# Optimization experiments

Hardware: AMD Instinct MI355X
Metric: run time of the kernel (lower is better)

The kernel has to match this reference:

```python
import jax, jax.numpy as jnp
import numpy as np

B, N, M, H = 32, 1024, 256, 128


def setup_inputs() -> dict:
    key = jax.random.key(0)
    kA, kh, kW1, kW2 = jax.random.split(key, 4)
    A = jax.random.uniform(kA, (B, N, N), dtype=jnp.float32)
    h = jax.random.normal(kh, (B, N, M), dtype=jnp.float32)
    # torch Linear default init scale ~ 1/sqrt(fan_in)
    W1 = jax.random.normal(kW1, (M, H), dtype=jnp.float32) / np.sqrt(M)
    b1 = jnp.zeros((H,), dtype=jnp.float32)
    W2 = jax.random.normal(kW2, (H, M), dtype=jnp.float32) / np.sqrt(H)
    b2 = jnp.zeros((M,), dtype=jnp.float32)
    return {"A": A, "h": h, "W1": W1, "b1": b1, "W2": W2, "b2": b2}


def reference(A, h, W1, b1, W2, b2):
    # k = bmm(A, h) / 3 : [B,N,M]
    k = jnp.einsum('bij,bjm->bim', A, h) / 3.0
    # eta_g: Linear -> ReLU -> Linear
    k = jax.nn.relu(k @ W1 + b1) @ W2 + b2
    # A_mask = max over last dim of A, keepdims -> [B,N,1]
    A_mask = jnp.max(A, axis=-1, keepdims=True)
    # gated combine: k*mask + h*(mask-1)*(-1) == k*mask + h*(1-mask)
    return k * A_mask + h * (1.0 - A_mask)
```

## Files before the change

kernel.cpp:

```cpp
#include <hip/hip_runtime.h>

typedef __attribute__((ext_vector_type(8))) short bf16x8;
typedef __attribute__((ext_vector_type(4))) float f32x4;
typedef __attribute__((ext_vector_type(8))) unsigned short u16x8;

#define BB 32
#define NN 1024
#define MM 256
#define HH 128

__device__ __forceinline__ unsigned short f2bf(float f) {
  union { float f; unsigned int u; } c; c.f = f;
  unsigned int u = c.u + 0x7fffu + ((c.u >> 16) & 1u);
  return (unsigned short)(u >> 16);
}

__device__ __forceinline__ unsigned int cvtpk(float lo, float hi) {
  unsigned int r;
  asm("v_cvt_pk_bf16_f32 %0, %1, %2" : "=v"(r) : "v"(lo), "v"(hi));
  return r;
}

__device__ __forceinline__ float4 gload_f4(const float* p) {
  float4 r;
  asm volatile("global_load_dwordx4 %0, %1, off" : "=v"(r) : "v"(p) : "memory");
  return r;
}

typedef __attribute__((address_space(3))) unsigned int as3_u32;
typedef const __attribute__((address_space(1))) unsigned int as1_u32;
__device__ __forceinline__ void gl_lds16(const void* g, void* l) {
  __builtin_amdgcn_global_load_lds((as1_u32*)g, (as3_u32*)l, 16, 0, 0);
}

__global__ __launch_bounds__(256)
void k_transpose_h(const float* __restrict__ hg, unsigned short* __restrict__ hTg) {
  __shared__ unsigned short tile[64][65];
  int bid = blockIdx.x;
  int b = bid >> 6;
  int t = bid & 63;
  int k0 = (t >> 2) << 6;
  int m0 = (t & 3) << 6;
  int tt = threadIdx.x;
  {
    int r = tt >> 2;
    int cg = (tt & 3) << 4;
    const float* src = hg + (((size_t)b * NN + k0 + r) * MM + m0 + cg);
#pragma unroll
    for (int i = 0; i < 4; ++i) {
      float4 v = reinterpret_cast<const float4*>(src)[i];
      tile[r][cg + i * 4 + 0] = f2bf(v.x);
      tile[r][cg + i * 4 + 1] = f2bf(v.y);
      tile[r][cg + i * 4 + 2] = f2bf(v.z);
      tile[r][cg + i * 4 + 3] = f2bf(v.w);
    }
  }
  __syncthreads();
  {
    int mr = tt >> 2;
    int kc = (tt & 3) << 4;
    alignas(16) unsigned short tmp[16];
#pragma unroll
    for (int i = 0; i < 16; ++i) tmp[i] = tile[kc + i][mr];
    unsigned short* dst = hTg + (((size_t)b * MM + m0 + mr) * NN + k0 + kc);
    *reinterpret_cast<u16x8*>(dst)     = *reinterpret_cast<u16x8*>(tmp);
    *reinterpret_cast<u16x8*>(dst + 8) = *reinterpret_cast<u16x8*>(tmp + 8);
  }
}

__global__ __launch_bounds__(256)
void k_transpose_w(const float* __restrict__ W1, const float* __restrict__ W2,
                   unsigned short* __restrict__ W1T, unsigned short* __restrict__ W2T) {
  int idx = blockIdx.x * 256 + threadIdx.x;
  if (idx < MM * HH) {
    int hc = idx >> 8;
    int m  = idx & 255;
    W1T[idx] = f2bf(W1[m * HH + hc]);
  } else {
    int j = idx - MM * HH;
    int m  = j >> 7;
    int hd = j & 127;
    W2T[j] = f2bf(W2[hd * MM + m]);
  }
}

#define AB0 0
#define AB1 16384
#define HB0 32768
#define HB1 65536
#define KLD 0
#define CLD 65536

#define PIPE_BARRIER() do { \
  asm volatile("s_waitcnt lgkmcnt(0)" ::: "memory"); \
  __builtin_amdgcn_s_barrier(); \
  asm volatile("" ::: "memory"); } while (0)

#define VMWAIT0() do { \
  asm volatile("s_waitcnt vmcnt(0)" ::: "memory"); \
  __builtin_amdgcn_sched_barrier(0); } while (0)

__global__ __launch_bounds__(512, 1)
void k_fused(const float* __restrict__ Ag, const float* __restrict__ hg,
             const unsigned short* __restrict__ hTg,
             const unsigned short* __restrict__ W1Tg,
             const unsigned short* __restrict__ W2Tg,
             const float* __restrict__ b1g, const float* __restrict__ b2g,
             float* __restrict__ outg) {
  __shared__ __align__(16) char smem[98304];
  __shared__ float smax[128];

  const int tid  = threadIdx.x;
  const int lane = tid & 63;
  const int wid  = tid >> 6;
  const int wr   = wid >> 2;
  const int wc   = wid & 3;
  const int l15  = lane & 15;
  const int lg   = lane >> 4;

  const int bid = blockIdx.x;
  const int b   = bid & 31;
  const int r0  = (bid >> 5) << 7;

  const float* Ab = Ag + ((size_t)b * NN + r0) * NN;
  const unsigned short* hTb = hTg + (size_t)b * MM * NN;

  const int arow = tid >> 2;
  const int acg  = (tid & 3) << 4;
  const int asw  = (arow & 7) << 4;
  const float* Asrc = Ab + (size_t)arow * NN + acg;

  const unsigned short* baseH[4];
#pragma unroll
  for (int i = 0; i < 4; ++i) {
    int c = i * 512 + tid;
    int col = c >> 3, cic = c & 7;
    baseH[i] = hTb + (size_t)col * NN + ((cic ^ (col & 7)) << 3);
  }
  const int ldsW = wid << 10;

#define STAGE_H(K0, HB)                                                     \
  do {                                                                      \
    _Pragma("unroll")                                                       \
    for (int i = 0; i < 4; ++i)                                             \
      gl_lds16(baseH[i] + (K0), smem + (HB) + ldsW + i * 8192);             \
  } while (0)

  float4 rA[4];
#define ISSUE_A(K0)                                                         \
  do {                                                                      \
    _Pragma("unroll")                                                       \
    for (int i = 0; i < 4; ++i) rA[i] = gload_f4(Asrc + (K0) + i * 4);      \
  } while (0)

  float pmax = -1e30f;
#define CVTWR(AB)                                                           \
  do {                                                                      \
    float m0 = fmaxf(fmaxf(rA[0].x, rA[0].y), fmaxf(rA[0].z, rA[0].w));     \
    float m1 = fmaxf(fmaxf(rA[1].x, rA[1].y), fmaxf(rA[1].z, rA[1].w));     \
    float m2 = fmaxf(fmaxf(rA[2].x, rA[2].y), fmaxf(rA[2].z, rA[2].w));     \
    float m3 = fmaxf(fmaxf(rA[3].x, rA[3].y), fmaxf(rA[3].z, rA[3].w));     \
    pmax = fmaxf(pmax, fmaxf(fmaxf(m0, m1), fmaxf(m2, m3)));                \
    uint4 q0 = make_uint4(cvtpk(rA[0].x, rA[0].y), cvtpk(rA[0].z, rA[0].w), \
                          cvtpk(rA[1].x, rA[1].y), cvtpk(rA[1].z, rA[1].w));\
    uint4 q1 = make_uint4(cvtpk(rA[2].x, rA[2].y), cvtpk(rA[2].z, rA[2].w), \
                          cvtpk(rA[3].x, rA[3].y), cvtpk(rA[3].z, rA[3].w));\
    *reinterpret_cast<uint4*>(smem + (AB) + arow * 128 + ((acg * 2) ^ asw)) = q0; \
    *reinterpret_cast<uint4*>(smem + (AB) + arow * 128 + ((acg * 2 + 16) ^ asw)) = q1; \
  } while (0)

  f32x4 acc[4][4];
#pragma unroll
  for (int m = 0; m < 4; ++m)
#pragma unroll
    for (int n = 0; n < 4; ++n) acc[m][n] = f32x4{0.f, 0.f, 0.f, 0.f};

#define CONSUME(AB, HB)                                                     \
  do {                                                                      \
    _Pragma("unroll")                                                       \
    for (int kk = 0; kk < 2; ++kk) {                                        \
      const int kb = (kk * 32 + (lg << 3)) * 2;                             \
      bf16x8 af[4], bh[4];                                                  \
      _Pragma("unroll")                                                     \
      for (int m = 0; m < 4; ++m) {                                         \
        int row = (wr << 6) + (m << 4) + l15;                               \
        af[m] = *reinterpret_cast<const bf16x8*>(                           \
            smem + (AB) + row * 128 + (kb ^ ((row & 7) << 4)));             \
      }                                                                     \
      _Pragma("unroll")                                                     \
      for (int n = 0; n < 4; ++n) {                                         \
        int col = (wc << 6) + (n << 4) + l15;                               \
        bh[n] = *reinterpret_cast<const bf16x8*>(                           \
            smem + (HB) + col * 128 + (kb ^ ((col & 7) << 4)));             \
      }                                                                     \
      _Pragma("unroll")                                                     \
      for (int m = 0; m < 4; ++m)                                           \
        _Pragma("unroll")                                                   \
        for (int n = 0; n < 4; ++n)                                         \
          acc[m][n] = __builtin_amdgcn_mfma_f32_16x16x32_bf16(af[m], bh[n], \
                                                              acc[m][n], 0, 0, 0); \
    }                                                                       \
  } while (0)

  ISSUE_A(0);
  STAGE_H(0, HB0);
  VMWAIT0();
  CVTWR(AB0);
  PIPE_BARRIER();

#pragma unroll
  for (int t = 0; t < 16; ++t) {
    if (t < 15) {
      ISSUE_A((t + 1) * 64);
      STAGE_H((t + 1) * 64, (t & 1) ? HB0 : HB1);
    }
    if (t & 1) CONSUME(AB1, HB1);
    else       CONSUME(AB0, HB0);
    if (t < 15) {
      VMWAIT0();
      if (t & 1) CVTWR(AB0);
      else       CVTWR(AB1);
      PIPE_BARRIER();
    }
  }

  {
    float v = pmax;
    v = fmaxf(v, __shfl_xor(v, 1));
    v = fmaxf(v, __shfl_xor(v, 2));
    if ((tid & 3) == 0) smax[arow] = v;
  }
  __syncthreads();

  {
    const float inv3 = 1.0f / 3.0f;
#pragma unroll
    for (int m = 0; m < 4; ++m)
#pragma unroll
      for (int n = 0; n < 4; ++n) {
        int col = (wc << 6) + (n << 4) + l15;
#pragma unroll
        for (int j = 0; j < 4; ++j) {
          int row = (wr << 6) + (m << 4) + (lg << 2) + j;
          *reinterpret_cast<unsigned short*>(smem + KLD + row * 512 +
                                             ((col * 2) ^ ((row & 7) << 4))) =
              f2bf(acc[m][n][j] * inv3);
        }
      }
  }
  __syncthreads();

  f32x4 acc1[4][2];
#pragma unroll
  for (int m = 0; m < 4; ++m)
#pragma unroll
    for (int n = 0; n < 2; ++n) acc1[m][n] = f32x4{0.f, 0.f, 0.f, 0.f};
  const int wcol1 = wc << 5;
#pragma unroll
  for (int kq = 0; kq < 8; ++kq) {
    bf16x8 af[4], bw[2];
#pragma unroll
    for (int m = 0; m < 4; ++m) {
      int row = (wr << 6) + (m << 4) + l15;
      af[m] = *reinterpret_cast<const bf16x8*>(smem + KLD + row * 512 +
              (((kq * 32 + (lg << 3)) * 2) ^ ((row & 7) << 4)));
    }
#pragma unroll
    for (int n = 0; n < 2; ++n) {
      int col = wcol1 + (n << 4) + l15;
      bw[n] = *reinterpret_cast<const bf16x8*>(W1Tg + (size_t)col * 256 +
                                               kq * 32 + (lg << 3));
    }
#pragma unroll
    for (int m = 0; m < 4; ++m)
#pragma unroll
      for (int n = 0; n < 2; ++n)
        acc1[m][n] = __builtin_amdgcn_mfma_f32_16x16x32_bf16(af[m], bw[n], acc1[m][n], 0, 0, 0);
  }

  {
#pragma unroll
    for (int n = 0; n < 2; ++n) {
      int col = wcol1 + (n << 4) + l15;
      float bias = b1g[col];
#pragma unroll
      for (int m = 0; m < 4; ++m)
#pragma unroll
        for (int j = 0; j < 4; ++j) {
          int row = (wr << 6) + (m << 4) + (lg << 2) + j;
          float v = fmaxf(acc1[m][n][j] + bias, 0.f);
          *reinterpret_cast<unsigned short*>(smem + CLD + row * 256 +
                                             ((col * 2) ^ ((row & 7) << 4))) = f2bf(v);
        }
    }
  }
  __syncthreads();

  f32x4 acc2[4][4];
#pragma unroll
  for (int m = 0; m < 4; ++m)
#pragma unroll
    for (int n = 0; n < 4; ++n) acc2[m][n] = f32x4{0.f, 0.f, 0.f, 0.f};
#pragma unroll
  for (int kq = 0; kq < 4; ++kq) {
    bf16x8 af[4], bw[4];
#pragma unroll
    for (int m = 0; m < 4; ++m) {
      int row = (wr << 6) + (m << 4) + l15;
      af[m] = *reinterpret_cast<const bf16x8*>(smem + CLD + row * 256 +
              (((kq * 32 + (lg << 3)) * 2) ^ ((row & 7) << 4)));
    }
#pragma unroll
    for (int n = 0; n < 4; ++n) {
      int col = (wc << 6) + (n << 4) + l15;
      bw[n] = *reinterpret_cast<const bf16x8*>(W2Tg + (size_t)col * 128 +
                                               kq * 32 + (lg << 3));
    }
#pragma unroll
    for (int m = 0; m < 4; ++m)
#pragma unroll
      for (int n = 0; n < 4; ++n)
        acc2[m][n] = __builtin_amdgcn_mfma_f32_16x16x32_bf16(af[m], bw[n], acc2[m][n], 0, 0, 0);
  }

  {
#pragma unroll
    for (int n = 0; n < 4; ++n) {
      int col = (wc << 6) + (n << 4) + l15;
      float b2v = b2g[col];
#pragma unroll
      for (int m = 0; m < 4; ++m)
#pragma unroll
        for (int j = 0; j < 4; ++j) {
          int row = (wr << 6) + (m << 4) + (lg << 2) + j;
          float kv = acc2[m][n][j] + b2v;
          float mask = smax[row];
          size_t gidx = ((size_t)b * NN + r0 + row) * MM + col;
          float hv = hg[gidx];
          outg[gidx] = kv * mask + hv * (1.f - mask);
        }
    }
  }
#undef CONSUME
#undef CVTWR
#undef ISSUE_A
#undef STAGE_H
}

extern "C" void kernel_launch(void* const* d_in, const int* in_sizes, int n_in,
                              void* d_out, int out_size, void* d_ws, size_t ws_size,
                              hipStream_t stream) {
  (void)in_sizes; (void)n_in; (void)out_size; (void)ws_size;
  const float* A  = (const float*)d_in[0];
  const float* h  = (const float*)d_in[1];
  const float* W1 = (const float*)d_in[2];
  const float* b1 = (const float*)d_in[3];
  const float* W2 = (const float*)d_in[4];
  const float* b2 = (const float*)d_in[5];
  float* out = (float*)d_out;

  unsigned short* hT  = (unsigned short*)d_ws;
  unsigned short* W1T = (unsigned short*)((char*)d_ws + (size_t)BB * MM * NN * 2);
  unsigned short* W2T = W1T + MM * HH;

  k_transpose_h<<<BB * 64, 256, 0, stream>>>(h, hT);
  k_transpose_w<<<256, 256, 0, stream>>>(W1, W2, W1T, W2T);
  k_fused<<<BB * 8, 512, 0, stream>>>(A, h, hT, W1T, W2T, b1, b2, out);
}
```

Baseline: 69.36 us.

## Halve K-tile, shrink LDS, two-stage register prefetch of A, merge prep kernels

The main GEMM loop now uses 32-wide K tiles instead of 64, which shrinks the LDS footprint from 96KB to 64KB and aliases the epilogue buffers onto offset 0. A is prefetched into two alternating register sets, so loads run two tiles ahead under partial vmcnt waits. The h and W transpose kernels are merged into a single launch, and the memory clobber is dropped from the asm global load. The aim is more latency hiding and one fewer launch, at the cost of twice as many barriers per K and an extra sync before the epilogue reuses LDS.

```diff
diff --git a/kernel.cpp b/kernel.cpp
--- a/kernel.cpp
+++ b/kernel.cpp
@@ -14,19 +14,16 @@
   unsigned int u = c.u + 0x7fffu + ((c.u >> 16) & 1u);
   return (unsigned short)(u >> 16);
 }
-
 __device__ __forceinline__ unsigned int cvtpk(float lo, float hi) {
   unsigned int r;
   asm("v_cvt_pk_bf16_f32 %0, %1, %2" : "=v"(r) : "v"(lo), "v"(hi));
   return r;
 }
-
 __device__ __forceinline__ float4 gload_f4(const float* p) {
   float4 r;
-  asm volatile("global_load_dwordx4 %0, %1, off" : "=v"(r) : "v"(p) : "memory");
+  asm volatile("global_load_dwordx4 %0, %1, off" : "=v"(r) : "v"(p));
   return r;
 }
-
 typedef __attribute__((address_space(3))) unsigned int as3_u32;
 typedef const __attribute__((address_space(1))) unsigned int as1_u32;
 __device__ __forceinline__ void gl_lds16(const void* g, void* l) {
@@ -34,80 +31,76 @@
 }
 
 __global__ __launch_bounds__(256)
-void k_transpose_h(const float* __restrict__ hg, unsigned short* __restrict__ hTg) {
-  __shared__ unsigned short tile[64][65];
+void k_prep(const float* __restrict__ hg, unsigned short* __restrict__ hTg,
+            const float* __restrict__ W1, const float* __restrict__ W2,
+            unsigned short* __restrict__ W1T, unsigned short* __restrict__ W2T) {
   int bid = blockIdx.x;
-  int b = bid >> 6;
-  int t = bid & 63;
-  int k0 = (t >> 2) << 6;
-  int m0 = (t & 3) << 6;
-  int tt = threadIdx.x;
-  {
-    int r = tt >> 2;
-    int cg = (tt & 3) << 4;
-    const float* src = hg + (((size_t)b * NN + k0 + r) * MM + m0 + cg);
-#pragma unroll
-    for (int i = 0; i < 4; ++i) {
-      float4 v = reinterpret_cast<const float4*>(src)[i];
-      tile[r][cg + i * 4 + 0] = f2bf(v.x);
-      tile[r][cg + i * 4 + 1] = f2bf(v.y);
-      tile[r][cg + i * 4 + 2] = f2bf(v.z);
-      tile[r][cg + i * 4 + 3] = f2bf(v.w);
-    }
-  }
-  __syncthreads();
-  {
-    int mr = tt >> 2;
-    int kc = (tt & 3) << 4;
-    alignas(16) unsigned short tmp[16];
-#pragma unroll
-    for (int i = 0; i < 16; ++i) tmp[i] = tile[kc + i][mr];
-    unsigned short* dst = hTg + (((size_t)b * MM + m0 + mr) * NN + k0 + kc);
-    *reinterpret_cast<u16x8*>(dst)     = *reinterpret_cast<u16x8*>(tmp);
-    *reinterpret_cast<u16x8*>(dst + 8) = *reinterpret_cast<u16x8*>(tmp + 8);
-  }
-}
-
-__global__ __launch_bounds__(256)
-void k_transpose_w(const float* __restrict__ W1, const float* __restrict__ W2,
-                   unsigned short* __restrict__ W1T, unsigned short* __restrict__ W2T) {
-  int idx = blockIdx.x * 256 + threadIdx.x;
-  if (idx < MM * HH) {
-    int hc = idx >> 8;
-    int m  = idx & 255;
-    W1T[idx] = f2bf(W1[m * HH + hc]);
+  if (bid < BB * 64) {
+    __shared__ unsigned short tile[64][65];
+    int b = bid >> 6;
+    int t = bid & 63;
+    int k0 = (t >> 2) << 6;
+    int m0 = (t & 3) << 6;
+    int tt = threadIdx.x;
+    {
+      int r = tt >> 2;
+      int cg = (tt & 3) << 4;
+      const float* src = hg + (((size_t)b * NN + k0 + r) * MM + m0 + cg);
+#pragma unroll
+      for (int i = 0; i < 4; ++i) {
+        float4 v = reinterpret_cast<const float4*>(src)[i];
+        tile[r][cg + i * 4 + 0] = f2bf(v.x);
+        tile[r][cg + i * 4 + 1] = f2bf(v.y);
+        tile[r][cg + i * 4 + 2] = f2bf(v.z);
+        tile[r][cg + i * 4 + 3] = f2bf(v.w);
+      }
+    }
+    __syncthreads();
+    {
+      int mr = tt >> 2;
+      int kc = (tt & 3) << 4;
+      alignas(16) unsigned short tmp[16];
+#pragma unroll
+      for (int i = 0; i < 16; ++i) tmp[i] = tile[kc + i][mr];
+      unsigned short* dst = hTg + (((size_t)b * MM + m0 + mr) * NN + k0 + kc);
+      *reinterpret_cast<u16x8*>(dst)     = *reinterpret_cast<u16x8*>(tmp);
+      *reinterpret_cast<u16x8*>(dst + 8) = *reinterpret_cast<u16x8*>(tmp + 8);
+    }
   } else {
-    int j = idx - MM * HH;
-    int m  = j >> 7;
-    int hd = j & 127;
-    W2T[j] = f2bf(W2[hd * MM + m]);
-  }
-}
-
-#define AB0 0
-#define AB1 16384
-#define HB0 32768
-#define HB1 65536
+    int idx = (bid - BB * 64) * 256 + threadIdx.x;
+    if (idx < MM * HH) {
+      int hc = idx >> 8;
+      int m  = idx & 255;
+      W1T[idx] = f2bf(W1[m * HH + hc]);
+    } else {
+      int j = idx - MM * HH;
+      int m  = j >> 7;
+      int hd = j & 127;
+      W2T[j] = f2bf(W2[hd * MM + m]);
+    }
+  }
+}
+
+#define AB_(x) ((x) * 8192)
+#define HB_(x) (16384 + (x) * 16384)
 #define KLD 0
-#define CLD 65536
+#define CLD 0
 
 #define PIPE_BARRIER() do { \
   asm volatile("s_waitcnt lgkmcnt(0)" ::: "memory"); \
   __builtin_amdgcn_s_barrier(); \
   asm volatile("" ::: "memory"); } while (0)
-
-#define VMWAIT0() do { \
-  asm volatile("s_waitcnt vmcnt(0)" ::: "memory"); \
+#define VMW(N) do { asm volatile("s_waitcnt vmcnt(" #N ")" ::: "memory"); \
   __builtin_amdgcn_sched_barrier(0); } while (0)
 
-__global__ __launch_bounds__(512, 1)
+__global__ __launch_bounds__(512, 4)
 void k_fused(const float* __restrict__ Ag, const float* __restrict__ hg,
              const unsigned short* __restrict__ hTg,
              const unsigned short* __restrict__ W1Tg,
              const unsigned short* __restrict__ W2Tg,
              const float* __restrict__ b1g, const float* __restrict__ b2g,
              float* __restrict__ outg) {
-  __shared__ __align__(16) char smem[98304];
+  __shared__ __align__(16) char smem[65536];
   __shared__ float smax[128];
 
   const int tid  = threadIdx.x;
@@ -126,100 +119,96 @@
   const unsigned short* hTb = hTg + (size_t)b * MM * NN;
 
   const int arow = tid >> 2;
-  const int acg  = (tid & 3) << 4;
-  const int asw  = (arow & 7) << 4;
-  const float* Asrc = Ab + (size_t)arow * NN + acg;
-
-  const unsigned short* baseH[4];
-#pragma unroll
-  for (int i = 0; i < 4; ++i) {
-    int c = i * 512 + tid;
-    int col = c >> 3, cic = c & 7;
-    baseH[i] = hTb + (size_t)col * NN + ((cic ^ (col & 7)) << 3);
-  }
-  const int ldsW = wid << 10;
-
-#define STAGE_H(K0, HB)                                                     \
-  do {                                                                      \
-    _Pragma("unroll")                                                       \
-    for (int i = 0; i < 4; ++i)                                             \
-      gl_lds16(baseH[i] + (K0), smem + (HB) + ldsW + i * 8192);             \
+  const int ass  = tid & 3;
+  const float* Asrc = Ab + (size_t)arow * NN + (ass << 3);
+  const int awb = arow * 64 + ((ass << 4) ^ ((arow & 3) << 4));
+
+  const unsigned short* baseH[2];
+  {
+    int c0 = tid;
+    baseH[0] = hTb + (size_t)(c0 >> 2) * NN + (((c0 & 3) ^ ((c0 >> 2) & 3)) << 3);
+    int c1 = tid + 512;
+    baseH[1] = hTb + (size_t)(c1 >> 2) * NN + (((c1 & 3) ^ ((c1 >> 2) & 3)) << 3);
+  }
+  const int dstW = wid << 10;
+
+#define STAGE_H(K0, HB)                                                      \
+  do {                                                                       \
+    gl_lds16(baseH[0] + (K0), smem + (HB) + dstW);                           \
+    gl_lds16(baseH[1] + (K0), smem + (HB) + 8192 + dstW);                    \
   } while (0)
 
-  float4 rA[4];
-#define ISSUE_A(K0)                                                         \
-  do {                                                                      \
-    _Pragma("unroll")                                                       \
-    for (int i = 0; i < 4; ++i) rA[i] = gload_f4(Asrc + (K0) + i * 4);      \
+  float4 xa0, xa1, ya0, ya1;
+#define ISSUE_AX(K0) do { xa0 = gload_f4(Asrc + (K0)); \
+                          xa1 = gload_f4(Asrc + (K0) + 4); } while (0)
+#define ISSUE_AY(K0) do { ya0 = gload_f4(Asrc + (K0)); \
+                          ya1 = gload_f4(Asrc + (K0) + 4); } while (0)
+
+  float pmax = -1e30f;
+#define CVTWR(AB, R0, R1)                                                    \
+  do {                                                                       \
+    pmax = fmaxf(pmax, fmaxf(fmaxf(fmaxf((R0).x, (R0).y), fmaxf((R0).z, (R0).w)), \
+                             fmaxf(fmaxf((R1).x, (R1).y), fmaxf((R1).z, (R1).w)))); \
+    uint2 q = make_uint2(cvtpk((R0).x, (R0).y), cvtpk((R0).z, (R0).w));      \
+    uint2 q2 = make_uint2(cvtpk((R1).x, (R1).y), cvtpk((R1).z, (R1).w));     \
+    *reinterpret_cast<uint2*>(smem + (AB) + awb)     = q;                    \
+    *reinterpret_cast<uint2*>(smem + (AB) + awb + 8) = q2;                   \
   } while (0)
 
-  float pmax = -1e30f;
-#define CVTWR(AB)                                                           \
-  do {                                                                      \
-    float m0 = fmaxf(fmaxf(rA[0].x, rA[0].y), fmaxf(rA[0].z, rA[0].w));     \
-    float m1 = fmaxf(fmaxf(rA[1].x, rA[1].y), fmaxf(rA[1].z, rA[1].w));     \
-    float m2 = fmaxf(fmaxf(rA[2].x, rA[2].y), fmaxf(rA[2].z, rA[2].w));     \
-    float m3 = fmaxf(fmaxf(rA[3].x, rA[3].y), fmaxf(rA[3].z, rA[3].w));     \
-    pmax = fmaxf(pmax, fmaxf(fmaxf(m0, m1), fmaxf(m2, m3)));                \
-    uint4 q0 = make_uint4(cvtpk(rA[0].x, rA[0].y), cvtpk(rA[0].z, rA[0].w), \
-                          cvtpk(rA[1].x, rA[1].y), cvtpk(rA[1].z, rA[1].w));\
-    uint4 q1 = make_uint4(cvtpk(rA[2].x, rA[2].y), cvtpk(rA[2].z, rA[2].w), \
-                          cvtpk(rA[3].x, rA[3].y), cvtpk(rA[3].z, rA[3].w));\
-    *reinterpret_cast<uint4*>(smem + (AB) + arow * 128 + ((acg * 2) ^ asw)) = q0; \
-    *reinterpret_cast<uint4*>(smem + (AB) + arow * 128 + ((acg * 2 + 16) ^ asw)) = q1; \
+  f32x4 acc[4][4];
+#pragma unroll
+  for (int m = 0; m < 4; ++m)
+#pragma unroll
+    for (int n = 0; n < 4; ++n) acc[m][n] = f32x4{0.f, 0.f, 0.f, 0.f};
+
+#define CONSUME(AB, HB)                                                      \
+  do {                                                                       \
+    bf16x8 af[4], bh[4];                                                     \
+    _Pragma("unroll")                                                        \
+    for (int m = 0; m < 4; ++m) {                                            \
+      int row = (wr << 6) + (m << 4) + l15;                                  \
+      af[m] = *reinterpret_cast<const bf16x8*>(                              \
+          smem + (AB) + row * 64 + ((lg << 4) ^ ((row & 3) << 4)));          \
+    }                                                                        \
+    _Pragma("unroll")                                                        \
+    for (int n = 0; n < 4; ++n) {                                            \
+      int col = (wc << 6) + (n << 4) + l15;                                  \
+      bh[n] = *reinterpret_cast<const bf16x8*>(                              \
+          smem + (HB) + col * 64 + ((lg << 4) ^ ((col & 3) << 4)));          \
+    }                                                                        \
+    _Pragma("unroll")                                                        \
+    for (int m = 0; m < 4; ++m)                                              \
+      _Pragma("unroll")                                                      \
+      for (int n = 0; n < 4; ++n)                                            \
+        acc[m][n] = __builtin_amdgcn_mfma_f32_16x16x32_bf16(af[m], bh[n],    \
+                                                            acc[m][n], 0, 0, 0); \
   } while (0)
 
-  f32x4 acc[4][4];
-#pragma unroll
-  for (int m = 0; m < 4; ++m)
-#pragma unroll
-    for (int n = 0; n < 4; ++n) acc[m][n] = f32x4{0.f, 0.f, 0.f, 0.f};
-
-#define CONSUME(AB, HB)                                                     \
-  do {                                                                      \
-    _Pragma("unroll")                                                       \
-    for (int kk = 0; kk < 2; ++kk) {                                        \
-      const int kb = (kk * 32 + (lg << 3)) * 2;                             \
-      bf16x8 af[4], bh[4];                                                  \
-      _Pragma("unroll")                                                     \
-      for (int m = 0; m < 4; ++m) {                                         \
-        int row = (wr << 6) + (m << 4) + l15;                               \
-        af[m] = *reinterpret_cast<const bf16x8*>(                           \
-            smem + (AB) + row * 128 + (kb ^ ((row & 7) << 4)));             \
-      }                                                                     \
-      _Pragma("unroll")                                                     \
-      for (int n = 0; n < 4; ++n) {                                         \
-        int col = (wc << 6) + (n << 4) + l15;                               \
-        bh[n] = *reinterpret_cast<const bf16x8*>(                           \
-            smem + (HB) + col * 128 + (kb ^ ((col & 7) << 4)));             \
-      }                                                                     \
-      _Pragma("unroll")                                                     \
-      for (int m = 0; m < 4; ++m)                                           \
-        _Pragma("unroll")                                                   \
-        for (int n = 0; n < 4; ++n)                                         \
-          acc[m][n] = __builtin_amdgcn_mfma_f32_16x16x32_bf16(af[m], bh[n], \
-                                                              acc[m][n], 0, 0, 0); \
-    }                                                                       \
-  } while (0)
-
-  ISSUE_A(0);
-  STAGE_H(0, HB0);
-  VMWAIT0();
-  CVTWR(AB0);
+  STAGE_H(0, HB_(0));
+  ISSUE_AY(0);
+  VMW(0);
+  CVTWR(AB_(0), ya0, ya1);
+  ISSUE_AX(32);
   PIPE_BARRIER();
 
 #pragma unroll
-  for (int t = 0; t < 16; ++t) {
-    if (t < 15) {
-      ISSUE_A((t + 1) * 64);
-      STAGE_H((t + 1) * 64, (t & 1) ? HB0 : HB1);
-    }
-    if (t & 1) CONSUME(AB1, HB1);
-    else       CONSUME(AB0, HB0);
-    if (t < 15) {
-      VMWAIT0();
-      if (t & 1) CVTWR(AB0);
-      else       CVTWR(AB1);
+  for (int t2 = 0; t2 < 16; ++t2) {
+    const int te = 2 * t2;
+    if (te < 31) STAGE_H((te + 1) * 32, HB_(1));
+    if (te < 30) ISSUE_AY((te + 2) * 32);
+    CONSUME(AB_(0), HB_(0));
+    if (te < 31) {
+      if (te < 30) VMW(2); else VMW(0);
+      CVTWR(AB_(1), xa0, xa1);
+      PIPE_BARRIER();
+    }
+    const int to = te + 1;
+    if (to < 31) STAGE_H((to + 1) * 32, HB_(0));
+    if (to < 30) ISSUE_AX((to + 2) * 32);
+    CONSUME(AB_(1), HB_(1));
+    if (to < 31) {
+      if (to < 30) VMW(2); else VMW(0);
+      CVTWR(AB_(0), ya0, ya1);
       PIPE_BARRIER();
     }
   }
@@ -277,6 +266,7 @@
       for (int n = 0; n < 2; ++n)
         acc1[m][n] = __builtin_amdgcn_mfma_f32_16x16x32_bf16(af[m], bw[n], acc1[m][n], 0, 0, 0);
   }
+  __syncthreads();
 
   {
 #pragma unroll
@@ -343,7 +333,8 @@
   }
 #undef CONSUME
 #undef CVTWR
-#undef ISSUE_A
+#undef ISSUE_AX
+#undef ISSUE_AY
 #undef STAGE_H
 }
 
@@ -363,7 +354,6 @@
   unsigned short* W1T = (unsigned short*)((char*)d_ws + (size_t)BB * MM * NN * 2);
   unsigned short* W2T = W1T + MM * HH;
 
-  k_transpose_h<<<BB * 64, 256, 0, stream>>>(h, hT);
-  k_transpose_w<<<256, 256, 0, stream>>>(W1, W2, W1T, W2T);
+  k_prep<<<BB * 64 + 256, 256, 0, stream>>>(h, hT, W1, W2, W1T, W2T);
   k_fused<<<BB * 8, 512, 0, stream>>>(A, h, hT, W1T, W2T, b1, b2, out);
 }
```

New measurement: 139.8 us. 2.02x slower.

## Coalesce A tile loads across rows, merge prep kernels, drop asm memory clobber

Applied to the files above, without the earlier changes.

The A-tile global load pattern changes so that 16 consecutive threads read one 256-byte row segment, giving contiguous coalesced loads. Each thread now covers four rows instead of one, which needs four partial row maxima and a 16-lane shuffle reduction. The two preprocessing kernels (h transpose and weight transpose) are merged into one launch to save a kernel launch. The memory clobber on the inline global load is removed, which gives the compiler more freedom to schedule but carries some ordering risk.

```diff
diff --git a/kernel.cpp b/kernel.cpp
--- a/kernel.cpp
+++ b/kernel.cpp
@@ -14,19 +14,16 @@
   unsigned int u = c.u + 0x7fffu + ((c.u >> 16) & 1u);
   return (unsigned short)(u >> 16);
 }
-
 __device__ __forceinline__ unsigned int cvtpk(float lo, float hi) {
   unsigned int r;
   asm("v_cvt_pk_bf16_f32 %0, %1, %2" : "=v"(r) : "v"(lo), "v"(hi));
   return r;
 }
-
 __device__ __forceinline__ float4 gload_f4(const float* p) {
   float4 r;
-  asm volatile("global_load_dwordx4 %0, %1, off" : "=v"(r) : "v"(p) : "memory");
+  asm volatile("global_load_dwordx4 %0, %1, off" : "=v"(r) : "v"(p));
   return r;
 }
-
 typedef __attribute__((address_space(3))) unsigned int as3_u32;
 typedef const __attribute__((address_space(1))) unsigned int as1_u32;
 __device__ __forceinline__ void gl_lds16(const void* g, void* l) {
@@ -34,53 +31,53 @@
 }
 
 __global__ __launch_bounds__(256)
-void k_transpose_h(const float* __restrict__ hg, unsigned short* __restrict__ hTg) {
-  __shared__ unsigned short tile[64][65];
+void k_prep(const float* __restrict__ hg, unsigned short* __restrict__ hTg,
+            const float* __restrict__ W1, const float* __restrict__ W2,
+            unsigned short* __restrict__ W1T, unsigned short* __restrict__ W2T) {
   int bid = blockIdx.x;
-  int b = bid >> 6;
-  int t = bid & 63;
-  int k0 = (t >> 2) << 6;
-  int m0 = (t & 3) << 6;
-  int tt = threadIdx.x;
-  {
-    int r = tt >> 2;
-    int cg = (tt & 3) << 4;
-    const float* src = hg + (((size_t)b * NN + k0 + r) * MM + m0 + cg);
-#pragma unroll
-    for (int i = 0; i < 4; ++i) {
-      float4 v = reinterpret_cast<const float4*>(src)[i];
-      tile[r][cg + i * 4 + 0] = f2bf(v.x);
-      tile[r][cg + i * 4 + 1] = f2bf(v.y);
-      tile[r][cg + i * 4 + 2] = f2bf(v.z);
-      tile[r][cg + i * 4 + 3] = f2bf(v.w);
-    }
-  }
-  __syncthreads();
-  {
-    int mr = tt >> 2;
-    int kc = (tt & 3) << 4;
-    alignas(16) unsigned short tmp[16];
-#pragma unroll
-    for (int i = 0; i < 16; ++i) tmp[i] = tile[kc + i][mr];
-    unsigned short* dst = hTg + (((size_t)b * MM + m0 + mr) * NN + k0 + kc);
-    *reinterpret_cast<u16x8*>(dst)     = *reinterpret_cast<u16x8*>(tmp);
-    *reinterpret_cast<u16x8*>(dst + 8) = *reinterpret_cast<u16x8*>(tmp + 8);
-  }
-}
-
-__global__ __launch_bounds__(256)
-void k_transpose_w(const float* __restrict__ W1, const float* __restrict__ W2,
-                   unsigned short* __restrict__ W1T, unsigned short* __restrict__ W2T) {
-  int idx = blockIdx.x * 256 + threadIdx.x;
-  if (idx < MM * HH) {
-    int hc = idx >> 8;
-    int m  = idx & 255;
-    W1T[idx] = f2bf(W1[m * HH + hc]);
+  if (bid < BB * 64) {
+    __shared__ unsigned short tile[64][65];
+    int b = bid >> 6;
+    int t = bid & 63;
+    int k0 = (t >> 2) << 6;
+    int m0 = (t & 3) << 6;
+    int tt = threadIdx.x;
+    {
+      int r = tt >> 2;
+      int cg = (tt & 3) << 4;
+      const float* src = hg + (((size_t)b * NN + k0 + r) * MM + m0 + cg);
+#pragma unroll
+      for (int i = 0; i < 4; ++i) {
+        float4 v = reinterpret_cast<const float4*>(src)[i];
+        tile[r][cg + i * 4 + 0] = f2bf(v.x);
+        tile[r][cg + i * 4 + 1] = f2bf(v.y);
+        tile[r][cg + i * 4 + 2] = f2bf(v.z);
+        tile[r][cg + i * 4 + 3] = f2bf(v.w);
+      }
+    }
+    __syncthreads();
+    {
+      int mr = tt >> 2;
+      int kc = (tt & 3) << 4;
+      alignas(16) unsigned short tmp[16];
+#pragma unroll
+      for (int i = 0; i < 16; ++i) tmp[i] = tile[kc + i][mr];
+      unsigned short* dst = hTg + (((size_t)b * MM + m0 + mr) * NN + k0 + kc);
+      *reinterpret_cast<u16x8*>(dst)     = *reinterpret_cast<u16x8*>(tmp);
+      *reinterpret_cast<u16x8*>(dst + 8) = *reinterpret_cast<u16x8*>(tmp + 8);
+    }
   } else {
-    int j = idx - MM * HH;
-    int m  = j >> 7;
-    int hd = j & 127;
-    W2T[j] = f2bf(W2[hd * MM + m]);
+    int idx = (bid - BB * 64) * 256 + threadIdx.x;
+    if (idx < MM * HH) {
+      int hc = idx >> 8;
+      int m  = idx & 255;
+      W1T[idx] = f2bf(W1[m * HH + hc]);
+    } else {
+      int j = idx - MM * HH;
+      int m  = j >> 7;
+      int hd = j & 127;
+      W2T[j] = f2bf(W2[hd * MM + m]);
+    }
   }
 }
 
@@ -125,10 +122,13 @@
   const float* Ab = Ag + ((size_t)b * NN + r0) * NN;
   const unsigned short* hTb = hTg + (size_t)b * MM * NN;
 
-  const int arow = tid >> 2;
-  const int acg  = (tid & 3) << 4;
-  const int asw  = (arow & 7) << 4;
-  const float* Asrc = Ab + (size_t)arow * NN + acg;
+  const int agrp = tid >> 4;
+  const int akc  = tid & 15;
+  const float* apA0 = Ab + (size_t)(agrp)      * NN + (akc << 2);
+  const float* apA1 = Ab + (size_t)(32 + agrp) * NN + (akc << 2);
+  const float* apA2 = Ab + (size_t)(64 + agrp) * NN + (akc << 2);
+  const float* apA3 = Ab + (size_t)(96 + agrp) * NN + (akc << 2);
+  const int asw = (agrp & 7) << 4;
 
   const unsigned short* baseH[4];
 #pragma unroll
@@ -146,27 +146,34 @@
       gl_lds16(baseH[i] + (K0), smem + (HB) + ldsW + i * 8192);             \
   } while (0)
 
-  float4 rA[4];
+  float4 rA0, rA1, rA2, rA3;
 #define ISSUE_A(K0)                                                         \
   do {                                                                      \
-    _Pragma("unroll")                                                       \
-    for (int i = 0; i < 4; ++i) rA[i] = gload_f4(Asrc + (K0) + i * 4);      \
+    rA0 = gload_f4(apA0 + (K0));                                            \
+    rA1 = gload_f4(apA1 + (K0));                                            \
+    rA2 = gload_f4(apA2 + (K0));                                            \
+    rA3 = gload_f4(apA3 + (K0));                                            \
   } while (0)
 
-  float pmax = -1e30f;
+  float pm0 = -1e30f, pm1 = -1e30f, pm2 = -1e30f, pm3 = -1e30f;
 #define CVTWR(AB)                                                           \
   do {                                                                      \
-    float m0 = fmaxf(fmaxf(rA[0].x, rA[0].y), fmaxf(rA[0].z, rA[0].w));     \
-    float m1 = fmaxf(fmaxf(rA[1].x, rA[1].y), fmaxf(rA[1].z, rA[1].w));     \
-    float m2 = fmaxf(fmaxf(rA[2].x, rA[2].y), fmaxf(rA[2].z, rA[2].w));     \
-    float m3 = fmaxf(fmaxf(rA[3].x, rA[3].y), fmaxf(rA[3].z, rA[3].w));     \
-    pmax = fmaxf(pmax, fmaxf(fmaxf(m0, m1), fmaxf(m2, m3)));                \
-    uint4 q0 = make_uint4(cvtpk(rA[0].x, rA[0].y), cvtpk(rA[0].z, rA[0].w), \
-                          cvtpk(rA[1].x, rA[1].y), cvtpk(rA[1].z, rA[1].w));\
-    uint4 q1 = make_uint4(cvtpk(rA[2].x, rA[2].y), cvtpk(rA[2].z, rA[2].w), \
-                          cvtpk(rA[3].x, rA[3].y), cvtpk(rA[3].z, rA[3].w));\
-    *reinterpret_cast<uint4*>(smem + (AB) + arow * 128 + ((acg * 2) ^ asw)) = q0; \
-    *reinterpret_cast<uint4*>(smem + (AB) + arow * 128 + ((acg * 2 + 16) ^ asw)) = q1; \
+    pm0 = fmaxf(pm0, fmaxf(fmaxf(rA0.x, rA0.y), fmaxf(rA0.z, rA0.w)));      \
+    pm1 = fmaxf(pm1, fmaxf(fmaxf(rA1.x, rA1.y), fmaxf(rA1.z, rA1.w)));      \
+    pm2 = fmaxf(pm2, fmaxf(fmaxf(rA2.x, rA2.y), fmaxf(rA2.z, rA2.w)));      \
+    pm3 = fmaxf(pm3, fmaxf(fmaxf(rA3.x, rA3.y), fmaxf(rA3.z, rA3.w)));      \
+    uint2 q0 = make_uint2(cvtpk(rA0.x, rA0.y), cvtpk(rA0.z, rA0.w));        \
+    uint2 q1 = make_uint2(cvtpk(rA1.x, rA1.y), cvtpk(rA1.z, rA1.w));        \
+    uint2 q2 = make_uint2(cvtpk(rA2.x, rA2.y), cvtpk(rA2.z, rA2.w));        \
+    uint2 q3 = make_uint2(cvtpk(rA3.x, rA3.y), cvtpk(rA3.z, rA3.w));        \
+    *reinterpret_cast<uint2*>(smem + (AB) + (agrp)      * 128 +             \
+                              (((akc << 3)) ^ asw)) = q0;                   \
+    *reinterpret_cast<uint2*>(smem + (AB) + (32 + agrp) * 128 +             \
+                              (((akc << 3)) ^ asw)) = q1;                   \
+    *reinterpret_cast<uint2*>(smem + (AB) + (64 + agrp) * 128 +             \
+                              (((akc << 3)) ^ asw)) = q2;                   \
+    *reinterpret_cast<uint2*>(smem + (AB) + (96 + agrp) * 128 +             \
+                              (((akc << 3)) ^ asw)) = q3;                   \
   } while (0)
 
   f32x4 acc[4][4];
@@ -225,10 +232,20 @@
   }
 
   {
-    float v = pmax;
-    v = fmaxf(v, __shfl_xor(v, 1));
-    v = fmaxf(v, __shfl_xor(v, 2));
-    if ((tid & 3) == 0) smax[arow] = v;
+    float v0 = pm0, v1 = pm1, v2 = pm2, v3 = pm3;
+#pragma unroll
+    for (int s = 1; s < 16; s <<= 1) {
+      v0 = fmaxf(v0, __shfl_xor(v0, s));
+      v1 = fmaxf(v1, __shfl_xor(v1, s));
+      v2 = fmaxf(v2, __shfl_xor(v2, s));
+      v3 = fmaxf(v3, __shfl_xor(v3, s));
+    }
+    if ((tid & 15) == 0) {
+      smax[agrp]      = v0;
+      smax[32 + agrp] = v1;
+      smax[64 + agrp] = v2;
+      smax[96 + agrp] = v3;
+    }
   }
   __syncthreads();
 
@@ -363,7 +380,6 @@
   unsigned short* W1T = (unsigned short*)((char*)d_ws + (size_t)BB * MM * NN * 2);
   unsigned short* W2T = W1T + MM * HH;
 
-  k_transpose_h<<<BB * 64, 256, 0, stream>>>(h, hT);
-  k_transpose_w<<<256, 256, 0, stream>>>(W1, W2, W1T, W2T);
+  k_prep<<<BB * 64 + 256, 256, 0, stream>>>(h, hT, W1, W2, W1T, W2T);
   k_fused<<<BB * 8, 512, 0, stream>>>(A, h, hT, W1T, W2T, b1, b2, out);
 }
```

New measurement: 63.19 us. 8.9% less time.
